# Kernel optimization log

Hardware: AMD Instinct MI355X
Metric: run time of the kernel (lower is better)

The kernel has to match this reference:

```python
import jax, jax.numpy as jnp
import numpy as np

OUT, IN = 16384, 4096
B, S = 4, 2048

def setup_inputs() -> dict:
    key = jax.random.key(0)
    k1, k2, k3, k4 = jax.random.split(key, 4)
    x = jax.random.normal(k1, (B, S, IN), dtype=jnp.float32)
    # int8 codes stored as int32 for harness compatibility; values in [-64, 63]
    weight_int8 = jax.random.randint(k2, (OUT, IN), 0, 127, dtype=jnp.int32) - 64
    scale = jax.random.uniform(k3, (OUT,), dtype=jnp.float32) * 0.01 + 1e-4
    bias = jax.random.normal(k4, (OUT,), dtype=jnp.float32)
    return {"x": x, "weight_int8": weight_int8, "scale": scale, "bias": bias}

def reference(x, weight_int8, scale, bias):
    # Dequantize: cast int8 codes to fp, apply per-row (per-out-channel) scale
    w = weight_int8.astype(x.dtype) * scale[:, None]          # [OUT, IN]
    # F.linear(x, W, b) = x @ W^T + b
    out = jnp.einsum('bsi,oi->bso', x, w) + bias               # [B, S, OUT]
    return out
```

## Files before the change

kernel.cpp:

```cpp
#include <hip/hip_runtime.h>
#include <hip/hip_bf16.h>
#include <stdint.h>
#include <stddef.h>

typedef __attribute__((ext_vector_type(8))) short  short8;
typedef __attribute__((ext_vector_type(4))) short  short4v;
typedef __attribute__((ext_vector_type(4))) float  floatx4;
typedef __attribute__((ext_vector_type(4))) int    int4v;

static constexpr int MDIM = 8192;
static constexpr int NDIM = 16384;
static constexpr int KDIM = 4096;
static constexpr int BM = 128, BN = 128, BK = 32;

__device__ __forceinline__ unsigned short f32_to_bf16_rne(float f) {
    union { float f; unsigned u; } v; v.f = f;
    unsigned r = v.u + 0x7fffu + ((v.u >> 16) & 1u);
    return (unsigned short)(r >> 16);
}


__global__ __launch_bounds__(256) void cvt_x_bf16(const float* __restrict__ x,
                                                  unsigned short* __restrict__ o) {
    size_t i = ((size_t)blockIdx.x * 256 + threadIdx.x) * 8;
    floatx4 a = *(const floatx4*)(x + i);
    floatx4 b = *(const floatx4*)(x + i + 4);
    short8 r;
    r[0] = (short)f32_to_bf16_rne(a[0]);
    r[1] = (short)f32_to_bf16_rne(a[1]);
    r[2] = (short)f32_to_bf16_rne(a[2]);
    r[3] = (short)f32_to_bf16_rne(a[3]);
    r[4] = (short)f32_to_bf16_rne(b[0]);
    r[5] = (short)f32_to_bf16_rne(b[1]);
    r[6] = (short)f32_to_bf16_rne(b[2]);
    r[7] = (short)f32_to_bf16_rne(b[3]);
    *(short8*)(o + i) = r;
}

__global__ __launch_bounds__(256) void cvt_w_bf16(const int* __restrict__ w,
                                                  unsigned short* __restrict__ o) {
    size_t i = ((size_t)blockIdx.x * 256 + threadIdx.x) * 8;
    int4v a = *(const int4v*)(w + i);
    int4v b = *(const int4v*)(w + i + 4);
    short8 r;
    r[0] = (short)f32_to_bf16_rne((float)a[0]);
    r[1] = (short)f32_to_bf16_rne((float)a[1]);
    r[2] = (short)f32_to_bf16_rne((float)a[2]);
    r[3] = (short)f32_to_bf16_rne((float)a[3]);
    r[4] = (short)f32_to_bf16_rne((float)b[0]);
    r[5] = (short)f32_to_bf16_rne((float)b[1]);
    r[6] = (short)f32_to_bf16_rne((float)b[2]);
    r[7] = (short)f32_to_bf16_rne((float)b[3]);
    *(short8*)(o + i) = r;
}


__device__ __forceinline__ void global_to_lds16(const unsigned short* g, unsigned short* l) {
    __builtin_amdgcn_global_load_lds(
        (__attribute__((address_space(1))) void*)(uintptr_t)g,
        (__attribute__((address_space(3))) void*)l,
        16, 0, 0);
}


__global__ __launch_bounds__(256) void gemm_bf16_bt(
        const unsigned short* __restrict__ A,
        const unsigned short* __restrict__ Bm,
        const float* __restrict__ scale,
        const float* __restrict__ bias,
        float* __restrict__ C) {
    __shared__ __align__(16) unsigned short sA[BM * BK];
    __shared__ __align__(16) unsigned short sB[BN * BK];

    const int tid = threadIdx.x;
    const int wv  = tid >> 6;
    const int ln  = tid & 63;
    const int bm  = blockIdx.y;
    const int bn  = blockIdx.x;
    const int wm  = wv >> 1;
    const int wn  = wv & 1;

    const int srow = wv * 16 + (ln >> 2);
    const int scol = (ln & 3) * 8;
    const unsigned short* gA0 = A  + (size_t)(bm * BM + srow) * KDIM + scol;
    const unsigned short* gA1 = gA0 + (size_t)64 * KDIM;
    const unsigned short* gB0 = Bm + (size_t)(bn * BN + srow) * KDIM + scol;
    const unsigned short* gB1 = gB0 + (size_t)64 * KDIM;
    unsigned short* lA0 = sA + (wv * 16) * BK;
    unsigned short* lA1 = sA + (64 + wv * 16) * BK;
    unsigned short* lB0 = sB + (wv * 16) * BK;
    unsigned short* lB1 = sB + (64 + wv * 16) * BK;

    const int aoff = (wm * 64 + (ln & 15)) * BK + (ln >> 4) * 8;
    const int boff = (wn * 64 + (ln & 15)) * BK + (ln >> 4) * 8;

    floatx4 acc[4][4];
    const floatx4 zero4 = {0.0f, 0.0f, 0.0f, 0.0f};
    #pragma unroll
    for (int i = 0; i < 4; ++i)
        #pragma unroll
        for (int j = 0; j < 4; ++j) acc[i][j] = zero4;

    for (int kt = 0; kt < KDIM; kt += BK) {
        global_to_lds16(gA0, lA0);
        global_to_lds16(gA1, lA1);
        global_to_lds16(gB0, lB0);
        global_to_lds16(gB1, lB1);
        gA0 += BK; gA1 += BK; gB0 += BK; gB1 += BK;
        __syncthreads();

        short8 af[4], bfr[4];
        #pragma unroll
        for (int t = 0; t < 4; ++t) {
            af[t]  = *(const short8*)(sA + aoff + t * 16 * BK);
            bfr[t] = *(const short8*)(sB + boff + t * 16 * BK);
        }
        #pragma unroll
        for (int mt = 0; mt < 4; ++mt)
            #pragma unroll
            for (int nt = 0; nt < 4; ++nt)
                acc[mt][nt] = __builtin_amdgcn_mfma_f32_16x16x32_bf16(
                    af[mt], bfr[nt], acc[mt][nt], 0, 0, 0);
        __syncthreads();
    }

    const int row0 = bm * BM + wm * 64 + (ln >> 4) * 4;
    const int col0 = bn * BN + wn * 64 + (ln & 15);
    #pragma unroll
    for (int nt = 0; nt < 4; ++nt) {
        const int col = col0 + nt * 16;
        const float sc = scale[col];
        const float bs = bias[col];
        #pragma unroll
        for (int mt = 0; mt < 4; ++mt) {
            float* cp = C + (size_t)(row0 + mt * 16) * NDIM + col;
            #pragma unroll
            for (int r = 0; r < 4; ++r)
                cp[(size_t)r * NDIM] = fmaf(acc[mt][nt][r], sc, bs);
        }
    }
}


__global__ __launch_bounds__(256) void gemm_fused(
        const float* __restrict__ A,
        const int* __restrict__ W,
        const float* __restrict__ scale,
        const float* __restrict__ bias,
        float* __restrict__ C) {
    __shared__ __align__(16) unsigned short sA[BM * BK];
    __shared__ __align__(16) unsigned short sB[BN * BK];

    const int tid = threadIdx.x;
    const int wv = tid >> 6, ln = tid & 63;
    const int bm = blockIdx.y, bn = blockIdx.x;
    const int wm = wv >> 1, wn = wv & 1;
    const int aoff = (wm * 64 + (ln & 15)) * BK + (ln >> 4) * 8;
    const int boff = (wn * 64 + (ln & 15)) * BK + (ln >> 4) * 8;

    floatx4 acc[4][4];
    const floatx4 zero4 = {0.0f, 0.0f, 0.0f, 0.0f};
    #pragma unroll
    for (int i = 0; i < 4; ++i)
        #pragma unroll
        for (int j = 0; j < 4; ++j) acc[i][j] = zero4;

    for (int kt = 0; kt < KDIM; kt += BK) {
        __syncthreads();
        #pragma unroll
        for (int j = 0; j < 4; ++j) {
            int u = tid + j * 256;
            int row = u >> 3;
            int c4 = (u & 7) * 4;
            floatx4 av = *(const floatx4*)(A + (size_t)(bm * BM + row) * KDIM + kt + c4);
            short4v as;
            as[0] = (short)f32_to_bf16_rne(av[0]);
            as[1] = (short)f32_to_bf16_rne(av[1]);
            as[2] = (short)f32_to_bf16_rne(av[2]);
            as[3] = (short)f32_to_bf16_rne(av[3]);
            *(short4v*)(sA + row * BK + c4) = as;
            int4v wq = *(const int4v*)(W + (size_t)(bn * BN + row) * KDIM + kt + c4);
            short4v bs;
            bs[0] = (short)f32_to_bf16_rne((float)wq[0]);
            bs[1] = (short)f32_to_bf16_rne((float)wq[1]);
            bs[2] = (short)f32_to_bf16_rne((float)wq[2]);
            bs[3] = (short)f32_to_bf16_rne((float)wq[3]);
            *(short4v*)(sB + row * BK + c4) = bs;
        }
        __syncthreads();

        short8 af[4], bfr[4];
        #pragma unroll
        for (int t = 0; t < 4; ++t) {
            af[t]  = *(const short8*)(sA + aoff + t * 16 * BK);
            bfr[t] = *(const short8*)(sB + boff + t * 16 * BK);
        }
        #pragma unroll
        for (int mt = 0; mt < 4; ++mt)
            #pragma unroll
            for (int nt = 0; nt < 4; ++nt)
                acc[mt][nt] = __builtin_amdgcn_mfma_f32_16x16x32_bf16(
                    af[mt], bfr[nt], acc[mt][nt], 0, 0, 0);
    }

    const int row0 = bm * BM + wm * 64 + (ln >> 4) * 4;
    const int col0 = bn * BN + wn * 64 + (ln & 15);
    #pragma unroll
    for (int nt = 0; nt < 4; ++nt) {
        const int col = col0 + nt * 16;
        const float sc = scale[col];
        const float bs = bias[col];
        #pragma unroll
        for (int mt = 0; mt < 4; ++mt) {
            float* cp = C + (size_t)(row0 + mt * 16) * NDIM + col;
            #pragma unroll
            for (int r = 0; r < 4; ++r)
                cp[(size_t)r * NDIM] = fmaf(acc[mt][nt][r], sc, bs);
        }
    }
}


extern "C" void kernel_launch(void* const* d_in, const int* in_sizes, int n_in,
                              void* d_out, int out_size, void* d_ws, size_t ws_size,
                              hipStream_t stream) {
    const float* x     = (const float*)d_in[0];
    const int*   w     = (const int*)d_in[1];
    const float* scale = (const float*)d_in[2];
    const float* bias  = (const float*)d_in[3];
    float* out = (float*)d_out;

    const size_t xElems = (size_t)MDIM * KDIM;
    const size_t wElems = (size_t)NDIM * KDIM;
    const size_t need   = (xElems + wElems) * sizeof(unsigned short);

    dim3 grid(NDIM / BN, MDIM / BM);

    if (ws_size >= need) {
        unsigned short* xb = (unsigned short*)d_ws;
        unsigned short* wb = xb + xElems;
        cvt_x_bf16<<<(unsigned)(xElems / (256 * 8)), 256, 0, stream>>>(x, xb);
        cvt_w_bf16<<<(unsigned)(wElems / (256 * 8)), 256, 0, stream>>>(w, wb);
        gemm_bf16_bt<<<grid, 256, 0, stream>>>(xb, wb, scale, bias, out);
    } else {
        gemm_fused<<<grid, 256, 0, stream>>>(x, w, scale, bias, out);
    }
}
```

Baseline: 1.991 ms.

## Replace bf16 GEMM with 256x256 tiled, 4-stage LDS pipelined kernel

Swaps the 128x128 single-buffered bf16 GEMM for a 512-thread kernel with 256x256 tiles. It runs a 4-stage ring of LDS buffers filled by direct global-to-LDS loads, waited on with explicit vmcnt counts and one barrier per K step. It also XOR-swizzles the LDS columns to avoid bank conflicts and remaps block order for L2 locality. The aim is to hide global load latency behind MFMA work and raise reuse per tile, at the cost of much more LDS (128KB) and register pressure.

```diff
diff --git a/kernel.cpp b/kernel.cpp
--- a/kernel.cpp
+++ b/kernel.cpp
@@ -11,7 +11,6 @@
 static constexpr int MDIM = 8192;
 static constexpr int NDIM = 16384;
 static constexpr int KDIM = 4096;
-static constexpr int BM = 128, BN = 128, BK = 32;
 
 __device__ __forceinline__ unsigned short f32_to_bf16_rne(float f) {
     union { float f; unsigned u; } v; v.f = f;
@@ -63,76 +62,104 @@
 }
 
 
-__global__ __launch_bounds__(256) void gemm_bf16_bt(
+static constexpr int BM2 = 256, BN2 = 256, BK2 = 32;
+
+#define PIPE_STAGE(SBUF)                                              \
+    do {                                                              \
+        global_to_lds16(pA0, &smem[SBUF][0][wid16][0]);               \
+        global_to_lds16(pA1, &smem[SBUF][0][128 + wid16][0]);         \
+        global_to_lds16(pB0, &smem[SBUF][1][wid16][0]);               \
+        global_to_lds16(pB1, &smem[SBUF][1][128 + wid16][0]);         \
+        pA0 += BK2; pA1 += BK2; pB0 += BK2; pB1 += BK2;               \
+    } while (0)
+
+#define PIPE_BODY(CBUF, SBUF, DO_STAGE, VM)                           \
+    do {                                                              \
+        if (DO_STAGE) { PIPE_STAGE(SBUF); }                           \
+        short8 af[8], bfr[4];                                         \
+        _Pragma("unroll")                                             \
+        for (int mt = 0; mt < 8; ++mt)                                \
+            af[mt] = *(const short8*)&smem[CBUF][0][arow + mt * 16][kcol]; \
+        _Pragma("unroll")                                             \
+        for (int nt = 0; nt < 4; ++nt)                                \
+            bfr[nt] = *(const short8*)&smem[CBUF][1][brow + nt * 16][kcol]; \
+        _Pragma("unroll")                                             \
+        for (int mt = 0; mt < 8; ++mt)                                \
+            _Pragma("unroll")                                         \
+            for (int nt = 0; nt < 4; ++nt)                            \
+                acc[mt][nt] = __builtin_amdgcn_mfma_f32_16x16x32_bf16(\
+                    af[mt], bfr[nt], acc[mt][nt], 0, 0, 0);           \
+        asm volatile("s_waitcnt vmcnt(" #VM ")" ::: "memory");        \
+        __builtin_amdgcn_s_barrier();                                 \
+        asm volatile("" ::: "memory");                                \
+    } while (0)
+
+__global__ __launch_bounds__(512, 2) void gemm_bf16_pipe(
         const unsigned short* __restrict__ A,
         const unsigned short* __restrict__ Bm,
         const float* __restrict__ scale,
         const float* __restrict__ bias,
         float* __restrict__ C) {
-    __shared__ __align__(16) unsigned short sA[BM * BK];
-    __shared__ __align__(16) unsigned short sB[BN * BK];
-
-    const int tid = threadIdx.x;
-    const int wv  = tid >> 6;
-    const int ln  = tid & 63;
-    const int bm  = blockIdx.y;
-    const int bn  = blockIdx.x;
-    const int wm  = wv >> 1;
-    const int wn  = wv & 1;
-
-    const int srow = wv * 16 + (ln >> 2);
-    const int scol = (ln & 3) * 8;
-    const unsigned short* gA0 = A  + (size_t)(bm * BM + srow) * KDIM + scol;
-    const unsigned short* gA1 = gA0 + (size_t)64 * KDIM;
-    const unsigned short* gB0 = Bm + (size_t)(bn * BN + srow) * KDIM + scol;
-    const unsigned short* gB1 = gB0 + (size_t)64 * KDIM;
-    unsigned short* lA0 = sA + (wv * 16) * BK;
-    unsigned short* lA1 = sA + (64 + wv * 16) * BK;
-    unsigned short* lB0 = sB + (wv * 16) * BK;
-    unsigned short* lB1 = sB + (64 + wv * 16) * BK;
-
-    const int aoff = (wm * 64 + (ln & 15)) * BK + (ln >> 4) * 8;
-    const int boff = (wn * 64 + (ln & 15)) * BK + (ln >> 4) * 8;
-
-    floatx4 acc[4][4];
+    __shared__ __align__(16) unsigned short smem[4][2][256][32];
+
+    const int tid   = threadIdx.x;
+    const int wid   = tid >> 6;
+    const int ln    = tid & 63;
+    const int wid16 = wid << 4;
+
+    const int lin = (int)blockIdx.x;
+    const int swz = (lin & 7) * 256 + (lin >> 3);
+    const int bm  = swz >> 6;
+    const int bn  = swz & 63;
+
+    const int wm = wid >> 2;
+    const int wn = wid & 3;
+
+    const int sr  = tid >> 2;
+    const int scc = ((tid & 3) * 8) ^ (((sr >> 1) & 3) << 3);
+    const unsigned short* pA0 = A  + (size_t)(bm * BM2 + sr) * KDIM + scc;
+    const unsigned short* pA1 = pA0 + (size_t)128 * KDIM;
+    const unsigned short* pB0 = Bm + (size_t)(bn * BN2 + sr) * KDIM + scc;
+    const unsigned short* pB1 = pB0 + (size_t)128 * KDIM;
+
+    const int arow = wm * 128 + (ln & 15);
+    const int brow = wn * 64  + (ln & 15);
+    const int kcol = ((ln >> 4) * 8) ^ ((((ln & 15) >> 1) & 3) << 3);
+
+    floatx4 acc[8][4];
     const floatx4 zero4 = {0.0f, 0.0f, 0.0f, 0.0f};
     #pragma unroll
-    for (int i = 0; i < 4; ++i)
+    for (int i = 0; i < 8; ++i)
         #pragma unroll
         for (int j = 0; j < 4; ++j) acc[i][j] = zero4;
 
-    for (int kt = 0; kt < KDIM; kt += BK) {
-        global_to_lds16(gA0, lA0);
-        global_to_lds16(gA1, lA1);
-        global_to_lds16(gB0, lB0);
-        global_to_lds16(gB1, lB1);
-        gA0 += BK; gA1 += BK; gB0 += BK; gB1 += BK;
-        __syncthreads();
-
-        short8 af[4], bfr[4];
-        #pragma unroll
-        for (int t = 0; t < 4; ++t) {
-            af[t]  = *(const short8*)(sA + aoff + t * 16 * BK);
-            bfr[t] = *(const short8*)(sB + boff + t * 16 * BK);
-        }
-        #pragma unroll
-        for (int mt = 0; mt < 4; ++mt)
-            #pragma unroll
-            for (int nt = 0; nt < 4; ++nt)
-                acc[mt][nt] = __builtin_amdgcn_mfma_f32_16x16x32_bf16(
-                    af[mt], bfr[nt], acc[mt][nt], 0, 0, 0);
-        __syncthreads();
-    }
-
-    const int row0 = bm * BM + wm * 64 + (ln >> 4) * 4;
-    const int col0 = bn * BN + wn * 64 + (ln & 15);
+    PIPE_STAGE(0);
+    PIPE_STAGE(1);
+    PIPE_STAGE(2);
+    asm volatile("s_waitcnt vmcnt(8)" ::: "memory");
+    __builtin_amdgcn_s_barrier();
+    asm volatile("" ::: "memory");
+
+    for (int it = 0; it < 31; ++it) {
+        PIPE_BODY(0, 3, true, 8);
+        PIPE_BODY(1, 0, true, 8);
+        PIPE_BODY(2, 1, true, 8);
+        PIPE_BODY(3, 2, true, 8);
+    }
+    PIPE_BODY(0, 3, true, 8);
+    PIPE_BODY(1, 0, false, 4);
+    PIPE_BODY(2, 0, false, 0);
+    PIPE_BODY(3, 0, false, 0);
+
+    const int row0 = bm * BM2 + wm * 128 + (ln >> 4) * 4;
+    const int col0 = bn * BN2 + wn * 64 + (ln & 15);
     #pragma unroll
     for (int nt = 0; nt < 4; ++nt) {
         const int col = col0 + nt * 16;
         const float sc = scale[col];
         const float bs = bias[col];
         #pragma unroll
-        for (int mt = 0; mt < 4; ++mt) {
+        for (int mt = 0; mt < 8; ++mt) {
             float* cp = C + (size_t)(row0 + mt * 16) * NDIM + col;
             #pragma unroll
             for (int r = 0; r < 4; ++r)
@@ -141,6 +168,8 @@
     }
 }
 
+
+static constexpr int BM = 128, BN = 128, BK = 32;
 
 __global__ __launch_bounds__(256) void gemm_fused(
         const float* __restrict__ A,
@@ -153,7 +182,7 @@
 
     const int tid = threadIdx.x;
     const int wv = tid >> 6, ln = tid & 63;
-    const int bm = blockIdx.y, bn = blockIdx.x;
+    const int bmi = blockIdx.y, bni = blockIdx.x;
     const int wm = wv >> 1, wn = wv & 1;
     const int aoff = (wm * 64 + (ln & 15)) * BK + (ln >> 4) * 8;
     const int boff = (wn * 64 + (ln & 15)) * BK + (ln >> 4) * 8;
@@ -172,14 +201,14 @@
             int u = tid + j * 256;
             int row = u >> 3;
             int c4 = (u & 7) * 4;
-            floatx4 av = *(const floatx4*)(A + (size_t)(bm * BM + row) * KDIM + kt + c4);
+            floatx4 av = *(const floatx4*)(A + (size_t)(bmi * BM + row) * KDIM + kt + c4);
             short4v as;
             as[0] = (short)f32_to_bf16_rne(av[0]);
             as[1] = (short)f32_to_bf16_rne(av[1]);
             as[2] = (short)f32_to_bf16_rne(av[2]);
             as[3] = (short)f32_to_bf16_rne(av[3]);
             *(short4v*)(sA + row * BK + c4) = as;
-            int4v wq = *(const int4v*)(W + (size_t)(bn * BN + row) * KDIM + kt + c4);
+            int4v wq = *(const int4v*)(W + (size_t)(bni * BN + row) * KDIM + kt + c4);
             short4v bs;
             bs[0] = (short)f32_to_bf16_rne((float)wq[0]);
             bs[1] = (short)f32_to_bf16_rne((float)wq[1]);
@@ -203,8 +232,8 @@
                     af[mt], bfr[nt], acc[mt][nt], 0, 0, 0);
     }
 
-    const int row0 = bm * BM + wm * 64 + (ln >> 4) * 4;
-    const int col0 = bn * BN + wn * 64 + (ln & 15);
+    const int row0 = bmi * BM + wm * 64 + (ln >> 4) * 4;
+    const int col0 = bni * BN + wn * 64 + (ln & 15);
     #pragma unroll
     for (int nt = 0; nt < 4; ++nt) {
         const int col = col0 + nt * 16;
@@ -234,15 +263,15 @@
     const size_t wElems = (size_t)NDIM * KDIM;
     const size_t need   = (xElems + wElems) * sizeof(unsigned short);
 
-    dim3 grid(NDIM / BN, MDIM / BM);
-
     if (ws_size >= need) {
         unsigned short* xb = (unsigned short*)d_ws;
         unsigned short* wb = xb + xElems;
         cvt_x_bf16<<<(unsigned)(xElems / (256 * 8)), 256, 0, stream>>>(x, xb);
         cvt_w_bf16<<<(unsigned)(wElems / (256 * 8)), 256, 0, stream>>>(w, wb);
-        gemm_bf16_bt<<<grid, 256, 0, stream>>>(xb, wb, scale, bias, out);
+        dim3 grid((MDIM / BM2) * (NDIM / BN2));
+        gemm_bf16_pipe<<<grid, 512, 0, stream>>>(xb, wb, scale, bias, out);
     } else {
+        dim3 grid(NDIM / BN, MDIM / BM);
         gemm_fused<<<grid, 256, 0, stream>>>(x, w, scale, bias, out);
     }
 }
```

Measured after the change: 1.781 ms. -10.5%, faster.
